# Optimization experiments

Hardware: AMD Instinct MI355X
Metric: run time of the kernel (lower is better)

Reference implementation:

```python
import jax, jax.numpy as jnp
import numpy as np

N = 100000
E = 1600000
G = 256
D_IN = 128
NEURON = 64
ATT_F = 8
K = 3
ALPHA = 0.1


def setup_inputs() -> dict:
    key = jax.random.key(0)
    ks = jax.random.split(key, 12)
    x = jax.random.normal(ks[0], (N, D_IN), dtype=jnp.float32)
    closeness_feature = jax.random.normal(ks[1], (N, ATT_F), dtype=jnp.float32)
    edge_index = jax.random.randint(ks[2], (2, E), 0, N, dtype=jnp.int32)
    batch = jnp.sort(jax.random.randint(ks[3], (N,), 0, G, dtype=jnp.int32))
    s = 0.05
    return {
        "x": x,
        "closeness_feature": closeness_feature,
        "edge_index": edge_index,
        "batch": batch,
        "num_graphs": G,
        "nn1_w": jax.random.normal(ks[4], (D_IN, NEURON), dtype=jnp.float32) * s,
        "nn1_b": jnp.zeros((NEURON,), dtype=jnp.float32),
        "close_w": jax.random.normal(ks[5], (ATT_F, 1), dtype=jnp.float32) * s,
        "close_b": jnp.zeros((1,), dtype=jnp.float32),
        "att1_w": jax.random.normal(ks[6], (NEURON, 16), dtype=jnp.float32) * s,
        "att1_b": jnp.zeros((16,), dtype=jnp.float32),
        "att2_w": jax.random.normal(ks[7], (16, 1), dtype=jnp.float32) * s,
        "att2_b": jnp.zeros((1,), dtype=jnp.float32),
    }


def _appnp(x, edge_index, n):
    # gcn_norm with self-loops: A_hat = D^{-1/2}(A+I)D^{-1/2}
    loop = jnp.arange(n, dtype=edge_index.dtype)
    src = jnp.concatenate([edge_index[0], loop])
    dst = jnp.concatenate([edge_index[1], loop])
    deg = jax.ops.segment_sum(jnp.ones_like(dst, dtype=x.dtype), dst, num_segments=n)
    dinv = jax.lax.rsqrt(deg)  # deg >= 1 due to self loops
    norm = (dinv[src] * dinv[dst])[:, None]  # [E+N, 1]
    h = x
    for _ in range(K):
        agg = jax.ops.segment_sum(norm * h[src], dst, num_segments=n)
        h = (1.0 - ALPHA) * agg + ALPHA * x
    return h


def reference(x, closeness_feature, edge_index, batch, num_graphs,
              nn1_w, nn1_b, close_w, close_b, att1_w, att1_b, att2_w, att2_b):
    n = x.shape[0]
    h = _appnp(x, edge_index, n)                      # [N, D_IN]
    h = jax.nn.relu(h @ nn1_w + nn1_b)                # [N, 64]

    # per-graph softmax over closeness scores (segment softmax)
    logits = (closeness_feature @ close_w + close_b)[:, 0]          # [N]
    m = jax.ops.segment_max(logits, batch, num_segments=num_graphs)  # [G]
    w = jnp.exp(logits - m[batch])
    z = jax.ops.segment_sum(w, batch, num_segments=num_graphs)       # [G]
    p = w / z[batch]                                                 # softmax per graph

    cnt = jax.ops.segment_sum(jnp.ones((n,), dtype=h.dtype), batch,
                              num_segments=num_graphs)               # nodes per graph
    p = p * cnt[batch]                                               # scaled by curr_size

    # self_max: per-graph max over weighted node features
    pooled = jax.ops.segment_max(p[:, None] * h, batch, num_segments=num_graphs)  # [G, 64]

    a = jax.nn.relu(pooled @ att1_w + att1_b)         # [G, 16]
    return a @ att2_w + att2_b                        # [G, 1]
```

## Files before the change

### kernel.cpp

```cpp
#include <hip/hip_runtime.h>
#include <cstdint>
#include <cstddef>


#define DIN 128
#define NEU 64
#define BK2 512
#define BKSHIFT2 9
#define BKCAP 16384
#define ESCAP 12288
#define MAXNB 256
#define ASTAGE 3200

typedef __attribute__((ext_vector_type(8))) short short8v;
typedef __attribute__((ext_vector_type(4))) float f32x4;

__device__ inline float bf2f(unsigned short h) {
    return __uint_as_float(((unsigned)h) << 16);
}
__device__ inline unsigned short f2bf(float f) {
    unsigned u = __float_as_uint(f);
    unsigned r = u + 0x7FFFu + ((u >> 16) & 1u);
    return (unsigned short)(r >> 16);
}


__global__ __launch_bounds__(256) void binA_fc1_kernel(
        const int* __restrict__ src, const int* __restrict__ dst,
        int* __restrict__ bcur, int* __restrict__ pk, int E, int NB, int nbinA,
        const float* __restrict__ x, const float* __restrict__ W,
        ushort* __restrict__ yb, int N) {
    __shared__ int smem[1280 + 2 * ASTAGE];
    int t = threadIdx.x;
    if ((int)blockIdx.x < nbinA) {
        int* hist   = smem;
        int* lstart = smem + 256;
        int* lcur   = smem + 512;
        int* resv   = smem + 768;
        int* sh     = smem + 1024;
        int* stage  = smem + 1280;
        int* gidx   = smem + 1280 + ASTAGE;
        int chunk = (E + nbinA - 1) / nbinA;
        int lo = blockIdx.x * chunk;
        int hi = min(E, lo + chunk);
        for (int b = t; b < NB; b += 256) hist[b] = 0;
        __syncthreads();
        for (int i = lo + t; i < hi; i += 256)
            atomicAdd(&hist[dst[i] >> BKSHIFT2], 1);
        __syncthreads();
        int c = (t < NB) ? hist[t] : 0;
        sh[t] = c;
        __syncthreads();
        for (int d = 1; d < 256; d <<= 1) {
            int u = (t >= d) ? sh[t - d] : 0;
            __syncthreads();
            sh[t] += u;
            __syncthreads();
        }
        if (t < NB) {
            int excl = sh[t] - c;
            lstart[t] = excl;
            lcur[t] = excl;
            resv[t] = atomicAdd(&bcur[t], c);
        }
        __syncthreads();
        for (int i = lo + t; i < hi; i += 256) {
            int d = dst[i], b = d >> BKSHIFT2;
            int p = atomicAdd(&lcur[b], 1);
            stage[p] = (src[i] << BKSHIFT2) | (d & (BK2 - 1));
            gidx[p] = resv[b] + (p - lstart[b]) + b * BKCAP;
        }
        __syncthreads();
        int total = hi - lo;
        for (int q = t; q < total; q += 256)
            pk[gidx[q]] = stage[q];
    } else {
        ushort* sW = (ushort*)smem;
        for (int k = t; k < DIN * NEU / 2; k += 256) {
            float2 v = ((const float2*)W)[k];
            ushort2 o;
            o.x = f2bf(v.x);
            o.y = f2bf(v.y);
            ((ushort2*)sW)[k] = o;
        }
        __syncthreads();
        int lane = t & 63;
        int wv = t >> 6;
        int l15 = lane & 15;
        int lg = lane >> 4;
        short8v bfrag[4][4];
#pragma unroll
        for (int kt = 0; kt < 4; kt++)
#pragma unroll
            for (int ct = 0; ct < 4; ct++) {
                short8v f;
#pragma unroll
                for (int e = 0; e < 8; e++)
                    f[e] = (short)sW[(kt * 32 + lg * 8 + e) * NEU + ct * 16 + l15];
                bfrag[kt][ct] = f;
            }
        long long row0 = (long long)(blockIdx.x - nbinA) * 64 + wv * 16;
        if (row0 >= N) return;
        bool rowok = (row0 + l15) < N;
        const float* xr = x + (size_t)(row0 + l15) * DIN;
        f32x4 acc[4];
#pragma unroll
        for (int ct = 0; ct < 4; ct++) acc[ct] = (f32x4){0.f, 0.f, 0.f, 0.f};
#pragma unroll
        for (int kt = 0; kt < 4; kt++) {
            short8v af = (short8v){0, 0, 0, 0, 0, 0, 0, 0};
            if (rowok) {
                float4 v0 = *((const float4*)(xr + kt * 32 + lg * 8));
                float4 v1 = *((const float4*)(xr + kt * 32 + lg * 8 + 4));
                af[0] = (short)f2bf(v0.x); af[1] = (short)f2bf(v0.y);
                af[2] = (short)f2bf(v0.z); af[3] = (short)f2bf(v0.w);
                af[4] = (short)f2bf(v1.x); af[5] = (short)f2bf(v1.y);
                af[6] = (short)f2bf(v1.z); af[7] = (short)f2bf(v1.w);
            }
#pragma unroll
            for (int ct = 0; ct < 4; ct++)
                acc[ct] = __builtin_amdgcn_mfma_f32_16x16x32_bf16(af, bfrag[kt][ct], acc[ct], 0, 0, 0);
        }
#pragma unroll
        for (int ct = 0; ct < 4; ct++)
#pragma unroll
            for (int r = 0; r < 4; r++) {
                long long rr = row0 + lg * 4 + r;
                if (rr < N) yb[(size_t)rr * NEU + ct * 16 + l15] = f2bf(acc[ct][r]);
            }
    }
}


__global__ __launch_bounds__(256) void binB_kernel(
        const int* __restrict__ bcur, const int* __restrict__ pk,
        int* __restrict__ es, int* __restrict__ rowptr,
        float* __restrict__ dinv, const ushort* __restrict__ yb,
        ushort* __restrict__ g0, int N, int NB) {
    __shared__ int cur[BK2];
    __shared__ int sh[256];
    __shared__ int esl[ESCAP];
    __shared__ int sbase[2];
    int b = blockIdx.x;
    int t = threadIdx.x;
    int node0 = b << BKSHIFT2;
    int v = (t < NB) ? bcur[t] : 0;
    sh[t] = v;
    __syncthreads();
    for (int d = 1; d < 256; d <<= 1) {
        int u = (t >= d) ? sh[t - d] : 0;
        __syncthreads();
        sh[t] += u;
        __syncthreads();
    }
    if (t == b) { sbase[0] = sh[t] - v; sbase[1] = v; }
    __syncthreads();
    int base = sbase[0];
    int count = sbase[1];
    const int* pb = pk + (size_t)b * BKCAP;

    for (int q = t; q < BK2; q += 256) cur[q] = 0;
    __syncthreads();
    for (int i = t; i < count; i += 256)
        atomicAdd(&cur[pb[i] & (BK2 - 1)], 1);
    __syncthreads();
    int c0 = cur[2 * t], c1 = cur[2 * t + 1];
    int s = c0 + c1;
    float dv0 = rsqrtf((float)c0 + 1.0f);
    float dv1 = rsqrtf((float)c1 + 1.0f);
    __syncthreads();
    sh[t] = s;
    __syncthreads();
    for (int d = 1; d < 256; d <<= 1) {
        int u = (t >= d) ? sh[t - d] : 0;
        __syncthreads();
        sh[t] += u;
        __syncthreads();
    }
    int excl = sh[t] - s;
    int n0 = node0 + 2 * t;
    if (n0 < N) {
        rowptr[n0 + 1] = base + excl + c0;
        dinv[n0] = dv0;
    }
    if (n0 + 1 < N) {
        rowptr[n0 + 2] = base + excl + c0 + c1;
        dinv[n0 + 1] = dv1;
    }
    if (b == 0 && t == 0) rowptr[0] = 0;
    __syncthreads();
    cur[2 * t] = excl;
    cur[2 * t + 1] = excl + c0;
    __syncthreads();
    for (int i = t; i < count; i += 256) {
        int w = pb[i];
        int pos = atomicAdd(&cur[w & (BK2 - 1)], 1);
        if (pos < ESCAP) esl[pos] = w >> BKSHIFT2;
    }
    __syncthreads();
    for (int i = t; i < count; i += 256) es[base + i] = esl[i];
    __syncthreads();
    float* fdinv = (float*)cur;
    fdinv[2 * t] = dv0;
    fdinv[2 * t + 1] = dv1;
    __syncthreads();
    for (int q = t; q < BK2 * 16; q += 256) {
        int ln = q >> 4, el = q & 15;
        int n = node0 + ln;
        if (n < N) {
            float dv = fdinv[ln];
            ushort4 w = *((const ushort4*)(yb + (size_t)n * NEU) + el);
            ushort4 o;
            o.x = f2bf(dv * bf2f(w.x));
            o.y = f2bf(dv * bf2f(w.y));
            o.z = f2bf(dv * bf2f(w.z));
            o.w = f2bf(dv * bf2f(w.w));
            *((ushort4*)(g0 + (size_t)n * NEU) + el) = o;
        }
    }
}


__device__ inline void acc4(float4& a, ushort4 w) {
    a.x += bf2f(w.x); a.y += bf2f(w.y); a.z += bf2f(w.z); a.w += bf2f(w.w);
}

template <int MODE>
__global__ __launch_bounds__(256) void pull_kernel(
        const int* __restrict__ rowptr, const int* __restrict__ es,
        const float* __restrict__ dinv, const ushort* __restrict__ gin,
        const ushort* __restrict__ yb, const float* __restrict__ b1,
        ushort* __restrict__ gout, float* __restrict__ h2out, int N) {
    int wid = threadIdx.x >> 6;
    int lane = threadIdx.x & 63;
    int quarter = lane >> 4;
    int l16 = lane & 15;
    int node = blockIdx.x * 4 + wid;
    if (node >= N) return;
    int beg = rowptr[node], end = rowptr[node + 1];
    float dd = dinv[node];
    const ushort4* gin4 = (const ushort4*)gin;
    float4 a0 = make_float4(0.f, 0.f, 0.f, 0.f);
    float4 a1 = make_float4(0.f, 0.f, 0.f, 0.f);
    int e = beg + quarter;
    for (; e + 4 < end; e += 8) {
        int s0 = es[e];
        int s1 = es[e + 4];
        ushort4 w0 = gin4[(uint)(s0 << 4) + l16];
        ushort4 w1 = gin4[(uint)(s1 << 4) + l16];
        acc4(a0, w0);
        acc4(a1, w1);
    }
    if (e < end) {
        int s0 = es[e];
        ushort4 w0 = gin4[(uint)(s0 << 4) + l16];
        acc4(a0, w0);
    }
    float4 acc;
    acc.x = a0.x + a1.x;
    acc.y = a0.y + a1.y;
    acc.z = a0.z + a1.z;
    acc.w = a0.w + a1.w;
    acc.x += __shfl_xor(acc.x, 16);
    acc.y += __shfl_xor(acc.y, 16);
    acc.z += __shfl_xor(acc.z, 16);
    acc.w += __shfl_xor(acc.w, 16);
    acc.x += __shfl_xor(acc.x, 32);
    acc.y += __shfl_xor(acc.y, 32);
    acc.z += __shfl_xor(acc.z, 32);
    acc.w += __shfl_xor(acc.w, 32);
    if (quarter == 0) {
        ushort4 gv = *((const ushort4*)(gin + (size_t)node * NEU) + l16);
        ushort4 yv = *((const ushort4*)(yb + (size_t)node * NEU) + l16);
        float c9 = 0.9f * dd;
        float hx = c9 * (acc.x + bf2f(gv.x)) + 0.1f * bf2f(yv.x);
        float hy = c9 * (acc.y + bf2f(gv.y)) + 0.1f * bf2f(yv.y);
        float hz = c9 * (acc.z + bf2f(gv.z)) + 0.1f * bf2f(yv.z);
        float hw = c9 * (acc.w + bf2f(gv.w)) + 0.1f * bf2f(yv.w);
        if (MODE == 1) {
            float4 bb = *((const float4*)b1 + l16);
            float4 o;
            o.x = fmaxf(hx + bb.x, 0.f);
            o.y = fmaxf(hy + bb.y, 0.f);
            o.z = fmaxf(hz + bb.z, 0.f);
            o.w = fmaxf(hw + bb.w, 0.f);
            *((float4*)(h2out + (size_t)node * NEU) + l16) = o;
        } else {
            ushort4 o;
            o.x = f2bf(dd * hx); o.y = f2bf(dd * hy);
            o.z = f2bf(dd * hz); o.w = f2bf(dd * hw);
            *((ushort4*)(gout + (size_t)node * NEU) + l16) = o;
        }
    }
}


__global__ __launch_bounds__(256) void head_kernel(
        const int* __restrict__ batch, const float* __restrict__ cf,
        const float* __restrict__ cw, const float* __restrict__ cb,
        const float* __restrict__ h2, const float* __restrict__ aw1,
        const float* __restrict__ ab1, const float* __restrict__ aw2,
        const float* __restrict__ ab2, float* __restrict__ out, int N) {
    int g = blockIdx.x;
    int tid = threadIdx.x;
    __shared__ int sbound[2];
    __shared__ float redm[256];
    __shared__ float redz[256];
    __shared__ float pooled[64];
    __shared__ float sa[16];
    if (tid < 2) {
        int target = g + tid;
        int lo = 0, hi = N;
        while (lo < hi) {
            int mid = (lo + hi) >> 1;
            if (batch[mid] < target) lo = mid + 1; else hi = mid;
        }
        sbound[tid] = lo;
    }
    __syncthreads();
    int s0 = sbound[0], e0 = sbound[1];
    float w0 = cw[0], w1 = cw[1], w2 = cw[2], w3 = cw[3];
    float w4 = cw[4], w5 = cw[5], w6 = cw[6], w7 = cw[7];
    float cb0 = cb[0];
    float m = -INFINITY, z = 0.f;
    for (int i = s0 + tid; i < e0; i += 256) {
        const float4* c = (const float4*)(cf + (size_t)i * 8);
        float4 A = c[0], B = c[1];
        float l = A.x * w0 + A.y * w1 + A.z * w2 + A.w * w3
                + B.x * w4 + B.y * w5 + B.z * w6 + B.w * w7 + cb0;
        float mn = fmaxf(m, l);
        z = z * __expf(m - mn) + __expf(l - mn);
        m = mn;
    }
    redm[tid] = m; redz[tid] = z;
    __syncthreads();
    for (int w = 128; w > 0; w >>= 1) {
        if (tid < w) {
            float ma = redm[tid], mb = redm[tid + w];
            float za = redz[tid], zb = redz[tid + w];
            float mn = fmaxf(ma, mb);
            redz[tid] = (mn == -INFINITY) ? 0.f
                       : za * __expf(ma - mn) + zb * __expf(mb - mn);
            redm[tid] = mn;
        }
        __syncthreads();
    }
    float M = redm[0];
    float scale = (float)(e0 - s0) / redz[0];
    __syncthreads();
    int j = tid & 63, r = tid >> 6;
    float mx = -INFINITY;
    for (int i = s0 + r; i < e0; i += 4) {
        const float4* c = (const float4*)(cf + (size_t)i * 8);
        float4 A = c[0], B = c[1];
        float l = A.x * w0 + A.y * w1 + A.z * w2 + A.w * w3
                + B.x * w4 + B.y * w5 + B.z * w6 + B.w * w7 + cb0;
        float p = __expf(l - M) * scale;
        mx = fmaxf(mx, p * h2[(size_t)i * NEU + j]);
    }
    redm[tid] = mx;
    __syncthreads();
    if (r == 0)
        pooled[j] = fmaxf(fmaxf(redm[j], redm[64 + j]),
                          fmaxf(redm[128 + j], redm[192 + j]));
    __syncthreads();
    if (tid < 16) {
        float acc = ab1[tid];
#pragma unroll
        for (int k = 0; k < 64; k++) acc = fmaf(pooled[k], aw1[k * 16 + tid], acc);
        sa[tid] = fmaxf(acc, 0.f);
    }
    __syncthreads();
    if (tid == 0) {
        float o = ab2[0];
#pragma unroll
        for (int k = 0; k < 16; k++) o = fmaf(sa[k], aw2[k], o);
        out[g] = o;
    }
}


extern "C" void kernel_launch(void* const* d_in, const int* in_sizes, int n_in,
                              void* d_out, int out_size, void* d_ws, size_t ws_size,
                              hipStream_t stream) {
    const float* x       = (const float*)d_in[0];
    const float* cf      = (const float*)d_in[1];
    const int*   ei      = (const int*)d_in[2];
    const int*   batch   = (const int*)d_in[3];
    const float* nn1_w   = (const float*)d_in[5];
    const float* nn1_b   = (const float*)d_in[6];
    const float* close_w = (const float*)d_in[7];
    const float* close_b = (const float*)d_in[8];
    const float* att1_w  = (const float*)d_in[9];
    const float* att1_b  = (const float*)d_in[10];
    const float* att2_w  = (const float*)d_in[11];
    const float* att2_b  = (const float*)d_in[12];
    float* out = (float*)d_out;

    int N = in_sizes[0] / DIN;
    int E = in_sizes[2] / 2;
    int G = out_size;

    const int* src = ei;
    const int* dst = ei + E;

    char* w = (char*)d_ws;
    size_t off = 0;
    auto alloc = [&](size_t bytes) -> void* {
        void* ptr = w + off;
        off += (bytes + 511) & ~(size_t)511;
        return ptr;
    };
    int NB = (N + BK2 - 1) >> BKSHIFT2;
    int nbinA = (E + ASTAGE - 1) / ASTAGE;
    int fc1b = (N + 63) / 64;

    ushort* yb     = (ushort*)alloc((size_t)N * NEU * 2);
    ushort* g0     = (ushort*)alloc((size_t)N * NEU * 2);
    ushort* g1     = (ushort*)alloc((size_t)N * NEU * 2);
    ushort* g2     = (ushort*)alloc((size_t)N * NEU * 2);
    float* h2      = (float*)alloc((size_t)N * NEU * 4);
    float* dinv    = (float*)alloc((size_t)N * 4);
    int*   rowptr  = (int*)alloc(((size_t)N + 1) * 4);
    int*   es      = (int*)alloc((size_t)E * 4);
    int*   bcur    = (int*)alloc((size_t)NB * 4);
    int*   pk      = (int*)alloc((size_t)NB * BKCAP * 4);
    (void)ws_size; (void)n_in;

    hipMemsetAsync(bcur, 0, (size_t)NB * 4, stream);

    binA_fc1_kernel<<<nbinA + fc1b, 256, 0, stream>>>(
        src, dst, bcur, pk, E, NB, nbinA, x, nn1_w, yb, N);

    binB_kernel<<<NB, 256, 0, stream>>>(bcur, pk, es, rowptr, dinv, yb, g0, N, NB);

    pull_kernel<0><<<(N + 3) / 4, 256, 0, stream>>>(rowptr, es, dinv, g0, yb, nn1_b, g1, nullptr, N);
    pull_kernel<0><<<(N + 3) / 4, 256, 0, stream>>>(rowptr, es, dinv, g1, yb, nn1_b, g2, nullptr, N);
    pull_kernel<1><<<(N + 3) / 4, 256, 0, stream>>>(rowptr, es, dinv, g2, yb, nn1_b, nullptr, h2, N);

    head_kernel<<<G, 256, 0, stream>>>(batch, cf, close_w, close_b, h2,
                                       att1_w, att1_b, att2_w, att2_b, out, N);
}
```

Baseline: 263.3 us.

## Split fused binning/fc1 kernel into separate launches with larger edge chunks

The combined edge-binning and fc1 GEMM kernel is split into two kernels launched back to back. Binning now runs on a fixed grid of 256 blocks with 6400-edge staging buffers instead of 500 blocks of 3200. The fc1 kernel gets its own launch with a smaller shared-memory footprint. This avoids one kernel's oversized LDS allocation limiting occupancy for the other role, at the cost of an extra launch and no overlap between the two phases.

Measured after the change: 269.5 us. 1.02x slower.

```diff
diff --git a/kernel.cpp b/kernel.cpp
--- a/kernel.cpp
+++ b/kernel.cpp
@@ -10,7 +10,7 @@
 #define BKCAP 16384
 #define ESCAP 12288
 #define MAXNB 256
-#define ASTAGE 3200
+#define ASTAGE 6400
 
 typedef __attribute__((ext_vector_type(8))) short short8v;
 typedef __attribute__((ext_vector_type(4))) float f32x4;
@@ -25,110 +25,52 @@
 }
 
 
-__global__ __launch_bounds__(256) void binA_fc1_kernel(
+__global__ __launch_bounds__(256) void binA_kernel(
         const int* __restrict__ src, const int* __restrict__ dst,
-        int* __restrict__ bcur, int* __restrict__ pk, int E, int NB, int nbinA,
-        const float* __restrict__ x, const float* __restrict__ W,
-        ushort* __restrict__ yb, int N) {
-    __shared__ int smem[1280 + 2 * ASTAGE];
+        int* __restrict__ bcur, int* __restrict__ pk, int E, int NB) {
+    __shared__ int hist[MAXNB];
+    __shared__ int lstart[MAXNB];
+    __shared__ int lcur[MAXNB];
+    __shared__ int resv[MAXNB];
+    __shared__ int sh[256];
+    __shared__ int stage[ASTAGE];
+    __shared__ int gidx[ASTAGE];
+    int nchunk = gridDim.x;
+    int chunk = (E + nchunk - 1) / nchunk;
+    int lo = blockIdx.x * chunk;
+    int hi = min(E, lo + chunk);
     int t = threadIdx.x;
-    if ((int)blockIdx.x < nbinA) {
-        int* hist   = smem;
-        int* lstart = smem + 256;
-        int* lcur   = smem + 512;
-        int* resv   = smem + 768;
-        int* sh     = smem + 1024;
-        int* stage  = smem + 1280;
-        int* gidx   = smem + 1280 + ASTAGE;
-        int chunk = (E + nbinA - 1) / nbinA;
-        int lo = blockIdx.x * chunk;
-        int hi = min(E, lo + chunk);
-        for (int b = t; b < NB; b += 256) hist[b] = 0;
-        __syncthreads();
-        for (int i = lo + t; i < hi; i += 256)
-            atomicAdd(&hist[dst[i] >> BKSHIFT2], 1);
-        __syncthreads();
-        int c = (t < NB) ? hist[t] : 0;
-        sh[t] = c;
-        __syncthreads();
-        for (int d = 1; d < 256; d <<= 1) {
-            int u = (t >= d) ? sh[t - d] : 0;
-            __syncthreads();
-            sh[t] += u;
-            __syncthreads();
-        }
-        if (t < NB) {
-            int excl = sh[t] - c;
-            lstart[t] = excl;
-            lcur[t] = excl;
-            resv[t] = atomicAdd(&bcur[t], c);
-        }
-        __syncthreads();
-        for (int i = lo + t; i < hi; i += 256) {
-            int d = dst[i], b = d >> BKSHIFT2;
-            int p = atomicAdd(&lcur[b], 1);
-            stage[p] = (src[i] << BKSHIFT2) | (d & (BK2 - 1));
-            gidx[p] = resv[b] + (p - lstart[b]) + b * BKCAP;
-        }
-        __syncthreads();
-        int total = hi - lo;
-        for (int q = t; q < total; q += 256)
-            pk[gidx[q]] = stage[q];
-    } else {
-        ushort* sW = (ushort*)smem;
-        for (int k = t; k < DIN * NEU / 2; k += 256) {
-            float2 v = ((const float2*)W)[k];
-            ushort2 o;
-            o.x = f2bf(v.x);
-            o.y = f2bf(v.y);
-            ((ushort2*)sW)[k] = o;
-        }
-        __syncthreads();
-        int lane = t & 63;
-        int wv = t >> 6;
-        int l15 = lane & 15;
-        int lg = lane >> 4;
-        short8v bfrag[4][4];
-#pragma unroll
-        for (int kt = 0; kt < 4; kt++)
-#pragma unroll
-            for (int ct = 0; ct < 4; ct++) {
-                short8v f;
-#pragma unroll
-                for (int e = 0; e < 8; e++)
-                    f[e] = (short)sW[(kt * 32 + lg * 8 + e) * NEU + ct * 16 + l15];
-                bfrag[kt][ct] = f;
-            }
-        long long row0 = (long long)(blockIdx.x - nbinA) * 64 + wv * 16;
-        if (row0 >= N) return;
-        bool rowok = (row0 + l15) < N;
-        const float* xr = x + (size_t)(row0 + l15) * DIN;
-        f32x4 acc[4];
-#pragma unroll
-        for (int ct = 0; ct < 4; ct++) acc[ct] = (f32x4){0.f, 0.f, 0.f, 0.f};
-#pragma unroll
-        for (int kt = 0; kt < 4; kt++) {
-            short8v af = (short8v){0, 0, 0, 0, 0, 0, 0, 0};
-            if (rowok) {
-                float4 v0 = *((const float4*)(xr + kt * 32 + lg * 8));
-                float4 v1 = *((const float4*)(xr + kt * 32 + lg * 8 + 4));
-                af[0] = (short)f2bf(v0.x); af[1] = (short)f2bf(v0.y);
-                af[2] = (short)f2bf(v0.z); af[3] = (short)f2bf(v0.w);
-                af[4] = (short)f2bf(v1.x); af[5] = (short)f2bf(v1.y);
-                af[6] = (short)f2bf(v1.z); af[7] = (short)f2bf(v1.w);
-            }
-#pragma unroll
-            for (int ct = 0; ct < 4; ct++)
-                acc[ct] = __builtin_amdgcn_mfma_f32_16x16x32_bf16(af, bfrag[kt][ct], acc[ct], 0, 0, 0);
-        }
-#pragma unroll
-        for (int ct = 0; ct < 4; ct++)
-#pragma unroll
-            for (int r = 0; r < 4; r++) {
-                long long rr = row0 + lg * 4 + r;
-                if (rr < N) yb[(size_t)rr * NEU + ct * 16 + l15] = f2bf(acc[ct][r]);
-            }
-    }
+    for (int b = t; b < NB; b += 256) hist[b] = 0;
+    __syncthreads();
+    for (int i = lo + t; i < hi; i += 256)
+        atomicAdd(&hist[dst[i] >> BKSHIFT2], 1);
+    __syncthreads();
+    int c = (t < NB) ? hist[t] : 0;
+    sh[t] = c;
+    __syncthreads();
+    for (int d = 1; d < 256; d <<= 1) {
+        int u = (t >= d) ? sh[t - d] : 0;
+        __syncthreads();
+        sh[t] += u;
+        __syncthreads();
+    }
+    if (t < NB) {
+        int excl = sh[t] - c;
+        lstart[t] = excl;
+        lcur[t] = excl;
+        resv[t] = atomicAdd(&bcur[t], c);
+    }
+    __syncthreads();
+    for (int i = lo + t; i < hi; i += 256) {
+        int d = dst[i], b = d >> BKSHIFT2;
+        int p = atomicAdd(&lcur[b], 1);
+        stage[p] = (src[i] << BKSHIFT2) | (d & (BK2 - 1));
+        gidx[p] = resv[b] + (p - lstart[b]) + b * BKCAP;
+    }
+    __syncthreads();
+    int total = hi - lo;
+    for (int q = t; q < total; q += 256)
+        pk[gidx[q]] = stage[q];
 }
 
 
@@ -218,6 +160,66 @@
             *((ushort4*)(g0 + (size_t)n * NEU) + el) = o;
         }
     }
+}
+
+
+__global__ __launch_bounds__(256) void fc1_kernel(
+        const float* __restrict__ x, const float* __restrict__ W,
+        ushort* __restrict__ yb, int N) {
+    __shared__ ushort sW[DIN * NEU];
+    int tid = threadIdx.x;
+    for (int k = tid; k < DIN * NEU / 2; k += 256) {
+        float2 v = ((const float2*)W)[k];
+        ushort2 o;
+        o.x = f2bf(v.x);
+        o.y = f2bf(v.y);
+        ((ushort2*)sW)[k] = o;
+    }
+    __syncthreads();
+    int lane = tid & 63;
+    int wv = tid >> 6;
+    int l15 = lane & 15;
+    int lg = lane >> 4;
+    short8v bfrag[4][4];
+#pragma unroll
+    for (int kt = 0; kt < 4; kt++)
+#pragma unroll
+        for (int ct = 0; ct < 4; ct++) {
+            short8v f;
+#pragma unroll
+            for (int e = 0; e < 8; e++)
+                f[e] = (short)sW[(kt * 32 + lg * 8 + e) * NEU + ct * 16 + l15];
+            bfrag[kt][ct] = f;
+        }
+    long long row0 = (long long)blockIdx.x * 64 + wv * 16;
+    if (row0 >= N) return;
+    bool rowok = (row0 + l15) < N;
+    const float* xr = x + (size_t)(row0 + l15) * DIN;
+    f32x4 acc[4];
+#pragma unroll
+    for (int ct = 0; ct < 4; ct++) acc[ct] = (f32x4){0.f, 0.f, 0.f, 0.f};
+#pragma unroll
+    for (int kt = 0; kt < 4; kt++) {
+        short8v af = (short8v){0, 0, 0, 0, 0, 0, 0, 0};
+        if (rowok) {
+            float4 v0 = *((const float4*)(xr + kt * 32 + lg * 8));
+            float4 v1 = *((const float4*)(xr + kt * 32 + lg * 8 + 4));
+            af[0] = (short)f2bf(v0.x); af[1] = (short)f2bf(v0.y);
+            af[2] = (short)f2bf(v0.z); af[3] = (short)f2bf(v0.w);
+            af[4] = (short)f2bf(v1.x); af[5] = (short)f2bf(v1.y);
+            af[6] = (short)f2bf(v1.z); af[7] = (short)f2bf(v1.w);
+        }
+#pragma unroll
+        for (int ct = 0; ct < 4; ct++)
+            acc[ct] = __builtin_amdgcn_mfma_f32_16x16x32_bf16(af, bfrag[kt][ct], acc[ct], 0, 0, 0);
+    }
+#pragma unroll
+    for (int ct = 0; ct < 4; ct++)
+#pragma unroll
+        for (int r = 0; r < 4; r++) {
+            long long rr = row0 + lg * 4 + r;
+            if (rr < N) yb[(size_t)rr * NEU + ct * 16 + l15] = f2bf(acc[ct][r]);
+        }
 }
 
 
@@ -412,8 +414,6 @@
         return ptr;
     };
     int NB = (N + BK2 - 1) >> BKSHIFT2;
-    int nbinA = (E + ASTAGE - 1) / ASTAGE;
-    int fc1b = (N + 63) / 64;
 
     ushort* yb     = (ushort*)alloc((size_t)N * NEU * 2);
     ushort* g0     = (ushort*)alloc((size_t)N * NEU * 2);
@@ -429,9 +429,9 @@
 
     hipMemsetAsync(bcur, 0, (size_t)NB * 4, stream);
 
-    binA_fc1_kernel<<<nbinA + fc1b, 256, 0, stream>>>(
-        src, dst, bcur, pk, E, NB, nbinA, x, nn1_w, yb, N);
-
+    fc1_kernel<<<(N + 63) / 64, 256, 0, stream>>>(x, nn1_w, yb, N);
+
+    binA_kernel<<<256, 256, 0, stream>>>(src, dst, bcur, pk, E, NB);
     binB_kernel<<<NB, 256, 0, stream>>>(bcur, pk, es, rowptr, dinv, yb, g0, N, NB);
 
     pull_kernel<0><<<(N + 3) / 4, 256, 0, stream>>>(rowptr, es, dinv, g0, yb, nn1_b, g1, nullptr, N);
```
